# Kernel optimization log

Hardware: AMD Instinct MI355X
Metric: run time of the kernel (lower is better)

Reference implementation:

```python
import jax, jax.numpy as jnp
import numpy as np

EPS = 1e-5
K = 1  # kernel_size; forced to 1 by the module's channel bookkeeping (see notes)


def conv2d(x, w, stride=1, padding=0):
    return jax.lax.conv_general_dilated(
        x, w, (stride, stride), [(padding, padding), (padding, padding)],
        dimension_numbers=('NCHW', 'OIHW', 'NCHW'))


def bn_eval(x, g, b):
    # eval-mode BatchNorm2d with running_mean=0, running_var=1
    scale = g * np.float32(1.0 / np.sqrt(1.0 + EPS))
    return x * scale.reshape(1, -1, 1, 1) + b.reshape(1, -1, 1, 1)


def spdconv(x, w, g, b):
    # SPDConv: 2x2 space-to-depth -> conv (bias=False) -> BN -> SiLU
    s2d = jnp.concatenate([x[..., ::2, ::2], x[..., 1::2, ::2],
                           x[..., ::2, 1::2], x[..., 1::2, 1::2]], axis=1)
    return jax.nn.silu(bn_eval(conv2d(s2d, w), g, b))


def fourier_split(x):
    # Fourierforward(J=1): zero-pad to next pow2, rfft2, split low/high bands
    h, w = x.shape[-2], x.shape[-1]
    ph = 1 << int(np.ceil(np.log2(h)))
    pw = 1 << int(np.ceil(np.log2(w)))
    xp = jnp.pad(x, ((0, 0), (0, 0), (0, ph - h), (0, pw - w)))
    f = jnp.fft.rfft2(xp)
    low = f[:, :, :h // 2 + 1, :w // 2 + 1]
    high = f[:, :, h // 2 + 1:h + 1, :w // 2 + 1]
    return low.real, low.imag, high.real, high.imag


def sdi(x, w, b):
    # SDI1: per-sample (unbatched) 3x3 conv, then cumulative product over the batch dim
    y = conv2d(x, w, padding=1) + b.reshape(1, -1, 1, 1)
    return jnp.cumprod(y, axis=0)


def fourier_sdi(x, sdi_w, sdi_b, fuse_w, fuse_g, fuse_b):
    yl, y1, y2, y3 = fourier_split(x)
    parts = [sdi(t, sdi_w, sdi_b) for t in (yl, y1, y2, y3)]
    cat = jnp.concatenate(parts, axis=1)  # (b, 4, h', w')
    return jax.nn.silu(bn_eval(conv2d(cat, fuse_w), fuse_g, fuse_b))


def _forward(x, w_spd_gw, bn_g_gw, bn_b_gw, sdi_w_gw, sdi_b_gw, fuse_w_gw, fuse_g_gw, fuse_b_gw,
             w_spd_gf, bn_g_gf, bn_b_gf, sdi_w_gf, sdi_b_gf, fuse_w_gf, fuse_g_gf, fuse_b_gf,
             gen_g, gen_b, w_final):
    b, c = x.shape[0], x.shape[1]
    # get_weight branch: SPDConv(1x1) -> Fourier_SDIModel
    weight = fourier_sdi(spdconv(x, w_spd_gw, bn_g_gw, bn_b_gw),
                         sdi_w_gw, sdi_b_gw, fuse_w_gw, fuse_g_gw, fuse_b_gw)
    h, w = weight.shape[2], weight.shape[3]
    weighted = jax.nn.softmax(weight.reshape(b, c * c, K * K, h, w), axis=2)
    # generate_feature branch: SPDConv(k) -> Fourier_SDIModel -> BN -> ReLU
    feat = fourier_sdi(spdconv(x, w_spd_gf, bn_g_gf, bn_b_gf),
                       sdi_w_gf, sdi_b_gf, fuse_w_gf, fuse_g_gf, fuse_b_gf)
    feat = jax.nn.relu(bn_eval(feat, gen_g, gen_b)).reshape(b, c * c, K * K, h, w)
    wd = feat * weighted
    # rearrange 'b c (n1 n2) h w -> b c (h n1) (w n2)'
    conv_data = wd.reshape(b, c * c, K, K, h, w).transpose(0, 1, 4, 2, 5, 3)
    conv_data = conv_data.reshape(b, c * c, h * K, w * K)
    # final conv: kernel K, stride autopad(K, p=K)=K (passed as stride arg), no bias
    return conv2d(conv_data, w_final, stride=K)


def setup_inputs() -> dict:
    key = jax.random.key(0)
    ks = jax.random.split(key, 24)
    n = lambda i, shape, s=1.0: jax.random.normal(ks[i], shape, dtype=jnp.float32) * s
    # sdi 3x3 weights scaled ~1/(fft_magnitude*taps) so the cumulative product over
    # the batch dim stays in fp32 range.
    return {
        'x': n(0, (16, 1, 1022, 1022)),
        'w_spd_gw': n(1, (1, 4, 1, 1), 0.5),
        'bn_g_gw': 1.0 + n(2, (1,), 0.1),
        'bn_b_gw': n(3, (1,), 0.1),
        'sdi_w_gw': n(4, (1, 1, 3, 3), 5e-4),
        'sdi_b_gw': n(5, (1,), 0.01),
        'fuse_w_gw': n(6, (1, 4, 1, 1), 0.3),
        'fuse_g_gw': 1.0 + n(7, (1,), 0.1),
        'fuse_b_gw': n(8, (1,), 0.1),
        'w_spd_gf': n(9, (1, 4, 1, 1), 0.5),
        'bn_g_gf': 1.0 + n(10, (1,), 0.1),
        'bn_b_gf': n(11, (1,), 0.1),
        'sdi_w_gf': n(12, (1, 1, 3, 3), 5e-4),
        'sdi_b_gf': n(13, (1,), 0.01),
        'fuse_w_gf': n(14, (1, 4, 1, 1), 0.3),
        'fuse_g_gf': 1.0 + n(15, (1,), 0.1),
        'fuse_b_gf': n(16, (1,), 0.1),
        'gen_g': 1.0 + n(17, (1,), 0.1),
        'gen_b': n(18, (1,), 0.1),
        'w_final': n(19, (64, 1, 1, 1), 0.1),
    }


def reference(x, w_spd_gw, bn_g_gw, bn_b_gw, sdi_w_gw, sdi_b_gw, fuse_w_gw, fuse_g_gw, fuse_b_gw,
              w_spd_gf, bn_g_gf, bn_b_gf, sdi_w_gf, sdi_b_gf, fuse_w_gf, fuse_g_gf, fuse_b_gf,
              gen_g, gen_b, w_final):
    return _forward(x, w_spd_gw, bn_g_gw, bn_b_gw, sdi_w_gw, sdi_b_gw, fuse_w_gw, fuse_g_gw, fuse_b_gw,
                    w_spd_gf, bn_g_gf, bn_b_gf, sdi_w_gf, sdi_b_gf, fuse_w_gf, fuse_g_gf, fuse_b_gf,
                    gen_g, gen_b, w_final)
```

## Files before the change

kernel.cpp:

```cpp
#include <hip/hip_runtime.h>
#include <math.h>


#define PI_F 3.14159265358979323846f

__device__ __forceinline__ int brev9(int x) { return (int)(__brev((unsigned)x) >> 23); }

__device__ __forceinline__ void fft512_lds(float2* row, const float* twc,
                                           const float* tws, int l) {
    for (int s = 1; s <= 9; s++) {
        int half = 1 << (s - 1);
        int m = half << 1;
#pragma unroll
        for (int n = 0; n < 4; n++) {
            int bt  = n * 64 + l;
            int grp = bt >> (s - 1);
            int pos = bt & (half - 1);
            int i0  = grp * m + pos;
            int i1  = i0 + half;
            int ti  = pos << (9 - s);
            float cs = twc[ti], sn = tws[ti];
            float2 u = row[i0], v = row[i1];
            float tr  = v.x * cs - v.y * sn;
            float tim = v.x * sn + v.y * cs;
            row[i0] = make_float2(u.x + tr,  u.y + tim);
            row[i1] = make_float2(u.x - tr,  u.y - tim);
        }
        __syncthreads();
    }
}

__global__ __launch_bounds__(512) void fft_rows_spd(
        const float* __restrict__ x, const float* __restrict__ w4,
        const float* __restrict__ g1, const float* __restrict__ b1,
        float2* __restrict__ RT) {
    __shared__ float2 s[8][513];
    __shared__ float twc[256];
    __shared__ float tws[256];
    int t = threadIdx.x;
    if (t < 256) {
        float ang = -2.0f * PI_F * (float)t / 512.0f;
        float sn, cs; sincosf(ang, &sn, &cs);
        twc[t] = cs; tws[t] = sn;
    }
    int w = t >> 6, l = t & 63;
    int row = blockIdx.x * 8 + w;
    int b = row >> 9, yy = row & 511;
    float w0 = w4[0], w1 = w4[1], w2 = w4[2], w3 = w4[3];
    float scale = g1[0] * rsqrtf(1.0f + 1e-5f);
    float bias  = b1[0];
#pragma unroll
    for (int n = 0; n < 8; n++) {
        int p = n * 64 + l;
        float v = 0.f;
        if (yy < 511 && p < 511) {
            const float* r0 = x + ((size_t)b * 1022 + 2 * yy) * 1022 + 2 * p;
            float2 e = *(const float2*)r0;
            float2 o = *(const float2*)(r0 + 1022);
            v = w0 * e.x + w1 * o.x + w2 * e.y + w3 * o.y;
            v = v * scale + bias;
            v = v / (1.0f + expf(-v));
        }
        s[w][brev9(p)] = make_float2(v, 0.f);
    }
    __syncthreads();
    fft512_lds(s[w], twc, tws, l);
    int k = t >> 1, sub = t & 1;
    int y0 = (blockIdx.x & 63) * 8;
    float2* dst = RT + ((size_t)(b * 256 + k)) * 512 + y0 + sub * 4;
#pragma unroll
    for (int r = 0; r < 4; r++) dst[r] = s[sub * 4 + r][k];
}

__global__ __launch_bounds__(512) void fft_cols_k(
        const float2* __restrict__ RT, float* __restrict__ tpl) {
    __shared__ float2 s[8][513];
    __shared__ float twc[256];
    __shared__ float tws[256];
    int t = threadIdx.x;
    if (t < 256) {
        float ang = -2.0f * PI_F * (float)t / 512.0f;
        float sn, cs; sincosf(ang, &sn, &cs);
        twc[t] = cs; tws[t] = sn;
    }
    int w = t >> 6, l = t & 63;
    int b = blockIdx.x >> 5;
    int kx0 = (blockIdx.x & 31) * 8;
    const float2* src = RT + ((size_t)(b * 256 + kx0 + w)) * 512;
#pragma unroll
    for (int n = 0; n < 8; n++) {
        int yv = n * 64 + l;
        s[w][brev9(yv)] = src[yv];
    }
    __syncthreads();
    fft512_lds(s[w], twc, tws, l);
    const size_t plane = (size_t)16 * 256 * 256;
    int kx_off = t & 7;
    int kyg = t >> 3;
#pragma unroll
    for (int p = 0; p < 4; p++) {
        int ky = p * 64 + kyg;
        float2 lo = s[kx_off][ky];
        float2 hi = s[kx_off][ky + 256];
        size_t off = ((size_t)(b * 256 + ky)) * 256 + kx0 + kx_off;
        tpl[off]             = lo.x;
        tpl[plane + off]     = lo.y;
        tpl[2 * plane + off] = hi.x;
        tpl[3 * plane + off] = hi.y;
    }
}

__global__ void conv_y_k(const float* __restrict__ tpl,
                         const float* __restrict__ sdiw,
                         const float* __restrict__ sdib,
                         float* __restrict__ y) {
    int idx = blockIdx.x * 256 + threadIdx.x;
    int j = idx & 255, i = (idx >> 8) & 255;
    const float* base = tpl + ((size_t)(idx >> 16)) * 65536;
    float acc = sdib[0];
    float w9[9];
#pragma unroll
    for (int k = 0; k < 9; k++) w9[k] = sdiw[k];
#pragma unroll
    for (int di = 0; di < 3; di++) {
        int ii = i + di - 1;
        if (ii < 0 || ii > 255) continue;
        const float* rowp = base + (size_t)ii * 256;
#pragma unroll
        for (int dj = 0; dj < 3; dj++) {
            int jj = j + dj - 1;
            if (jj < 0 || jj > 255) continue;
            acc += w9[di * 3 + dj] * rowp[jj];
        }
    }
    y[idx] = acc;
}

__global__ void cum_fuse_k(const float* __restrict__ y,
                           const float* __restrict__ fw,
                           const float* __restrict__ fg,
                           const float* __restrict__ fb,
                           const float* __restrict__ gg,
                           const float* __restrict__ gb,
                           float* __restrict__ feat2) {
    int pix = blockIdx.x * 256 + threadIdx.x;
    float v[16][4];
#pragma unroll
    for (int b = 0; b < 16; b++)
#pragma unroll
        for (int c = 0; c < 4; c++)
            v[b][c] = y[((size_t)(c * 16 + b)) * 65536 + pix];
    float inv = rsqrtf(1.0f + 1e-5f);
    float fscale = fg[0] * inv, fbias = fb[0];
    float gscale = gg[0] * inv, gbias = gb[0];
    float fw0 = fw[0], fw1 = fw[1], fw2 = fw[2], fw3 = fw[3];
    float p0 = 1.f, p1 = 1.f, p2 = 1.f, p3 = 1.f;
#pragma unroll
    for (int b = 0; b < 16; b++) {
        p0 *= v[b][0]; p1 *= v[b][1]; p2 *= v[b][2]; p3 *= v[b][3];
        float f = fw0 * p0 + fw1 * p1 + fw2 * p2 + fw3 * p3;
        float bnv = f * fscale + fbias;
        float feat = bnv / (1.0f + expf(-bnv));
        float f2 = feat * gscale + gbias;
        f2 = fmaxf(f2, 0.f);
        feat2[(size_t)b * 65536 + pix] = f2;
    }
}

__global__ void expand_out(const float* __restrict__ feat2,
                           const float* __restrict__ wf,
                           float* __restrict__ out) {
    int tid = blockIdx.x * 256 + threadIdx.x;
    int j4 = tid & 63;
    int i  = (tid >> 6) & 255;
    int b  = tid >> 14;
    const float4 v = *(const float4*)(feat2 + (((size_t)b * 256 + i) * 256 + j4 * 4));
    float* obase = out + (size_t)b * 64 * 65536 + (size_t)i * 256 + j4 * 4;
#pragma unroll
    for (int o = 0; o < 64; o++) {
        float sC = wf[o];
        float4 r = make_float4(v.x * sC, v.y * sC, v.z * sC, v.w * sC);
        *(float4*)(obase + (size_t)o * 65536) = r;
    }
}

extern "C" void kernel_launch(void* const* d_in, const int* in_sizes, int n_in,
                              void* d_out, int out_size, void* d_ws, size_t ws_size,
                              hipStream_t stream) {
    const float* x    = (const float*)d_in[0];
    const float* wspd = (const float*)d_in[9];
    const float* bng  = (const float*)d_in[10];
    const float* bnb  = (const float*)d_in[11];
    const float* sdiw = (const float*)d_in[12];
    const float* sdib = (const float*)d_in[13];
    const float* fw   = (const float*)d_in[14];
    const float* fg   = (const float*)d_in[15];
    const float* fb   = (const float*)d_in[16];
    const float* gg   = (const float*)d_in[17];
    const float* gb   = (const float*)d_in[18];
    const float* wf   = (const float*)d_in[19];
    float* out = (float*)d_out;

    float2* RT    = (float2*)d_ws;
    float*  tpl   = (float*)d_ws + (size_t)4 * 1024 * 1024;
    float*  y     = (float*)d_ws;
    float*  feat2 = tpl;

    fft_rows_spd<<<dim3(1024),  dim3(512), 0, stream>>>(x, wspd, bng, bnb, RT);
    fft_cols_k  <<<dim3(512),   dim3(512), 0, stream>>>(RT, tpl);
    conv_y_k    <<<dim3(16384), dim3(256), 0, stream>>>(tpl, sdiw, sdib, y);
    cum_fuse_k  <<<dim3(256),   dim3(256), 0, stream>>>(y, fw, fg, fb, gg, gb, feat2);
    expand_out  <<<dim3(1024),  dim3(256), 0, stream>>>(feat2, wf, out);
}
```

Baseline: 414.2 us.

## Use register radix-8 FFT and fuse cumulative product with output expansion

Replaces the LDS-based radix-2 512-point FFT (nine barrier-separated stages, with twiddle tables) with a three-pass radix-8 decomposition. Butterflies run in registers, twiddles come from sincosf, and only two LDS transposes are needed. The FFT outputs are staged through a padded shared tile so global stores are more contiguous. The cumulative-product/fuse kernel is merged with the 64-channel output expansion, which removes the intermediate feat2 buffer and one launch. The catch is that the fused kernel writes with only one float per thread per row, at 256-pixel granularity across 512 blocks, which may reduce store efficiency and parallelism for the dominant 268MB output write.

```diff
diff --git a/kernel.cpp b/kernel.cpp
--- a/kernel.cpp
+++ b/kernel.cpp
@@ -4,109 +4,168 @@
 
 #define PI_F 3.14159265358979323846f
 
-__device__ __forceinline__ int brev9(int x) { return (int)(__brev((unsigned)x) >> 23); }
-
-__device__ __forceinline__ void fft512_lds(float2* row, const float* twc,
-                                           const float* tws, int l) {
-    for (int s = 1; s <= 9; s++) {
-        int half = 1 << (s - 1);
-        int m = half << 1;
-#pragma unroll
-        for (int n = 0; n < 4; n++) {
-            int bt  = n * 64 + l;
-            int grp = bt >> (s - 1);
-            int pos = bt & (half - 1);
-            int i0  = grp * m + pos;
-            int i1  = i0 + half;
-            int ti  = pos << (9 - s);
-            float cs = twc[ti], sn = tws[ti];
-            float2 u = row[i0], v = row[i1];
-            float tr  = v.x * cs - v.y * sn;
-            float tim = v.x * sn + v.y * cs;
-            row[i0] = make_float2(u.x + tr,  u.y + tim);
-            row[i1] = make_float2(u.x - tr,  u.y - tim);
-        }
-        __syncthreads();
-    }
-}
-
-__global__ __launch_bounds__(512) void fft_rows_spd(
+struct cpx { float re, im; };
+__device__ __forceinline__ cpx cadd(cpx a, cpx b){ return {a.re+b.re, a.im+b.im}; }
+__device__ __forceinline__ cpx csub(cpx a, cpx b){ return {a.re-b.re, a.im-b.im}; }
+__device__ __forceinline__ cpx cmul(cpx a, cpx b){ return {a.re*b.re - a.im*b.im, a.re*b.im + a.im*b.re}; }
+__device__ __forceinline__ cpx cnegi(cpx a){ return {a.im, -a.re}; }
+
+__device__ __forceinline__ void dft8_dif(cpx* a) {
+    const float C = 0.70710678118654752440f;
+    cpx t0=cadd(a[0],a[4]), t1=cadd(a[1],a[5]), t2=cadd(a[2],a[6]), t3=cadd(a[3],a[7]);
+    cpx s0=csub(a[0],a[4]), s1=csub(a[1],a[5]), s2=csub(a[2],a[6]), s3=csub(a[3],a[7]);
+    s1 = (cpx){ C*(s1.re + s1.im), C*(s1.im - s1.re) };
+    s2 = cnegi(s2);
+    s3 = (cpx){ C*(s3.im - s3.re), -C*(s3.re + s3.im) };
+    cpx u0=cadd(t0,t2), u1=cadd(t1,t3), u2=csub(t0,t2), u3=cnegi(csub(t1,t3));
+    cpx v0=cadd(s0,s2), v1=cadd(s1,s3), v2=csub(s0,s2), v3=cnegi(csub(s1,s3));
+    a[0]=cadd(u0,u1); a[1]=csub(u0,u1); a[2]=cadd(u2,u3); a[3]=csub(u2,u3);
+    a[4]=cadd(v0,v1); a[5]=csub(v0,v1); a[6]=cadd(v2,v3); a[7]=csub(v2,v3);
+}
+
+__device__ __forceinline__ void twiddle_brev(cpx* a, cpx p) {
+    cpx w = p;
+    a[4] = cmul(a[4], w); w = cmul(w, p);
+    a[2] = cmul(a[2], w); w = cmul(w, p);
+    a[6] = cmul(a[6], w); w = cmul(w, p);
+    a[1] = cmul(a[1], w); w = cmul(w, p);
+    a[5] = cmul(a[5], w); w = cmul(w, p);
+    a[3] = cmul(a[3], w); w = cmul(w, p);
+    a[7] = cmul(a[7], w);
+}
+
+__device__ __forceinline__ void fft512_r8(cpx* a, float* bR, float* bI, int t) {
+    float sn, cs;
+    dft8_dif(a);
+    sincosf(-2.0f * PI_F * (float)t / 512.0f, &sn, &cs);
+    twiddle_brev(a, (cpx){cs, sn});
+    bR[0*69 + t] = a[0].re; bI[0*69 + t] = a[0].im;
+    bR[4*69 + t] = a[1].re; bI[4*69 + t] = a[1].im;
+    bR[2*69 + t] = a[2].re; bI[2*69 + t] = a[2].im;
+    bR[6*69 + t] = a[3].re; bI[6*69 + t] = a[3].im;
+    bR[1*69 + t] = a[4].re; bI[1*69 + t] = a[4].im;
+    bR[5*69 + t] = a[5].re; bI[5*69 + t] = a[5].im;
+    bR[3*69 + t] = a[6].re; bI[3*69 + t] = a[6].im;
+    bR[7*69 + t] = a[7].re; bI[7*69 + t] = a[7].im;
+    __syncthreads();
+    int k0 = t & 7, t0 = t >> 3;
+    cpx b[8];
+#pragma unroll
+    for (int i = 0; i < 8; i++) {
+        b[i].re = bR[k0*69 + t0 + 8*i];
+        b[i].im = bI[k0*69 + t0 + 8*i];
+    }
+    __syncthreads();
+    dft8_dif(b);
+    sincosf(-2.0f * PI_F * (float)t0 / 64.0f, &sn, &cs);
+    twiddle_brev(b, (cpx){cs, sn});
+    bR[(0*8 + k0)*9 + t0] = b[0].re; bI[(0*8 + k0)*9 + t0] = b[0].im;
+    bR[(4*8 + k0)*9 + t0] = b[1].re; bI[(4*8 + k0)*9 + t0] = b[1].im;
+    bR[(2*8 + k0)*9 + t0] = b[2].re; bI[(2*8 + k0)*9 + t0] = b[2].im;
+    bR[(6*8 + k0)*9 + t0] = b[3].re; bI[(6*8 + k0)*9 + t0] = b[3].im;
+    bR[(1*8 + k0)*9 + t0] = b[4].re; bI[(1*8 + k0)*9 + t0] = b[4].im;
+    bR[(5*8 + k0)*9 + t0] = b[5].re; bI[(5*8 + k0)*9 + t0] = b[5].im;
+    bR[(3*8 + k0)*9 + t0] = b[6].re; bI[(3*8 + k0)*9 + t0] = b[6].im;
+    bR[(7*8 + k0)*9 + t0] = b[7].re; bI[(7*8 + k0)*9 + t0] = b[7].im;
+    __syncthreads();
+    int rowb = ((t >> 3) * 8 + (t & 7)) * 9;
+#pragma unroll
+    for (int i = 0; i < 8; i++) {
+        a[i].re = bR[rowb + i];
+        a[i].im = bI[rowb + i];
+    }
+    __syncthreads();
+    dft8_dif(a);
+}
+
+__global__ __launch_bounds__(512) void fft_rows_spd8(
         const float* __restrict__ x, const float* __restrict__ w4,
         const float* __restrict__ g1, const float* __restrict__ b1,
         float2* __restrict__ RT) {
-    __shared__ float2 s[8][513];
-    __shared__ float twc[256];
-    __shared__ float tws[256];
-    int t = threadIdx.x;
-    if (t < 256) {
-        float ang = -2.0f * PI_F * (float)t / 512.0f;
-        float sn, cs; sincosf(ang, &sn, &cs);
-        twc[t] = cs; tws[t] = sn;
-    }
-    int w = t >> 6, l = t & 63;
+    __shared__ __align__(16) float pool[9216];
+    int tid = threadIdx.x;
+    int w = tid >> 6, t = tid & 63;
+    float* bR = pool + w * 1152;
+    float* bI = bR + 576;
     int row = blockIdx.x * 8 + w;
     int b = row >> 9, yy = row & 511;
-    float w0 = w4[0], w1 = w4[1], w2 = w4[2], w3 = w4[3];
-    float scale = g1[0] * rsqrtf(1.0f + 1e-5f);
+    float w0 = w4[0], w1 = w4[1], w2c = w4[2], w3 = w4[3];
+    float scale = g1[0] * rsqrtf(1.f + 1e-5f);
     float bias  = b1[0];
-#pragma unroll
-    for (int n = 0; n < 8; n++) {
-        int p = n * 64 + l;
+    cpx a[8];
+#pragma unroll
+    for (int m = 0; m < 8; m++) {
+        int p = t + 64 * m;
         float v = 0.f;
         if (yy < 511 && p < 511) {
             const float* r0 = x + ((size_t)b * 1022 + 2 * yy) * 1022 + 2 * p;
             float2 e = *(const float2*)r0;
             float2 o = *(const float2*)(r0 + 1022);
-            v = w0 * e.x + w1 * o.x + w2 * e.y + w3 * o.y;
+            v = w0 * e.x + w1 * o.x + w2c * e.y + w3 * o.y;
             v = v * scale + bias;
-            v = v / (1.0f + expf(-v));
+            v = v / (1.f + expf(-v));
         }
-        s[w][brev9(p)] = make_float2(v, 0.f);
-    }
-    __syncthreads();
-    fft512_lds(s[w], twc, tws, l);
-    int k = t >> 1, sub = t & 1;
+        a[m] = (cpx){v, 0.f};
+    }
+    fft512_r8(a, bR, bI, t);
+    float2* tile = (float2*)pool;
+    tile[(t +   0) * 9 + w] = make_float2(a[0].re, a[0].im);
+    tile[(t +  64) * 9 + w] = make_float2(a[4].re, a[4].im);
+    tile[(t + 128) * 9 + w] = make_float2(a[2].re, a[2].im);
+    tile[(t + 192) * 9 + w] = make_float2(a[6].re, a[6].im);
+    __syncthreads();
     int y0 = (blockIdx.x & 63) * 8;
-    float2* dst = RT + ((size_t)(b * 256 + k)) * 512 + y0 + sub * 4;
-#pragma unroll
-    for (int r = 0; r < 4; r++) dst[r] = s[sub * 4 + r][k];
-}
-
-__global__ __launch_bounds__(512) void fft_cols_k(
+    float2* dst = RT + (size_t)(b * 256) * 512 + y0;
+#pragma unroll
+    for (int r = 0; r < 4; r++) {
+        int e = tid + 512 * r;
+        int k = e >> 3, ww = e & 7;
+        dst[(size_t)k * 512 + ww] = tile[k * 9 + ww];
+    }
+}
+
+__global__ __launch_bounds__(512) void fft_cols8(
         const float2* __restrict__ RT, float* __restrict__ tpl) {
-    __shared__ float2 s[8][513];
-    __shared__ float twc[256];
-    __shared__ float tws[256];
-    int t = threadIdx.x;
-    if (t < 256) {
-        float ang = -2.0f * PI_F * (float)t / 512.0f;
-        float sn, cs; sincosf(ang, &sn, &cs);
-        twc[t] = cs; tws[t] = sn;
-    }
-    int w = t >> 6, l = t & 63;
+    __shared__ __align__(16) float pool[9216];
+    int tid = threadIdx.x;
+    int w = tid >> 6, t = tid & 63;
+    float* bR = pool + w * 1152;
+    float* bI = bR + 576;
     int b = blockIdx.x >> 5;
     int kx0 = (blockIdx.x & 31) * 8;
-    const float2* src = RT + ((size_t)(b * 256 + kx0 + w)) * 512;
-#pragma unroll
-    for (int n = 0; n < 8; n++) {
-        int yv = n * 64 + l;
-        s[w][brev9(yv)] = src[yv];
-    }
-    __syncthreads();
-    fft512_lds(s[w], twc, tws, l);
-    const size_t plane = (size_t)16 * 256 * 256;
-    int kx_off = t & 7;
-    int kyg = t >> 3;
-#pragma unroll
-    for (int p = 0; p < 4; p++) {
-        int ky = p * 64 + kyg;
-        float2 lo = s[kx_off][ky];
-        float2 hi = s[kx_off][ky + 256];
-        size_t off = ((size_t)(b * 256 + ky)) * 256 + kx0 + kx_off;
-        tpl[off]             = lo.x;
-        tpl[plane + off]     = lo.y;
-        tpl[2 * plane + off] = hi.x;
-        tpl[3 * plane + off] = hi.y;
+    const float2* src = RT + (size_t)(b * 256 + kx0 + w) * 512;
+    cpx a[8];
+#pragma unroll
+    for (int m = 0; m < 8; m++) {
+        float2 v = src[t + 64 * m];
+        a[m] = (cpx){v.x, v.y};
+    }
+    fft512_r8(a, bR, bI, t);
+    float2* tile = (float2*)pool;
+    tile[(t +   0) * 9 + w] = make_float2(a[0].re, a[0].im);
+    tile[(t +  64) * 9 + w] = make_float2(a[4].re, a[4].im);
+    tile[(t + 128) * 9 + w] = make_float2(a[2].re, a[2].im);
+    tile[(t + 192) * 9 + w] = make_float2(a[6].re, a[6].im);
+    tile[(t + 256) * 9 + w] = make_float2(a[1].re, a[1].im);
+    tile[(t + 320) * 9 + w] = make_float2(a[5].re, a[5].im);
+    tile[(t + 384) * 9 + w] = make_float2(a[3].re, a[3].im);
+    tile[(t + 448) * 9 + w] = make_float2(a[7].re, a[7].im);
+    __syncthreads();
+    const size_t P = (size_t)16 * 256 * 256;
+#pragma unroll
+    for (int r = 0; r < 8; r++) {
+        int e = tid + 512 * r;
+        int ky = e >> 3, ww = e & 7;
+        float2 v = tile[ky * 9 + ww];
+        if (ky < 256) {
+            size_t idx = (size_t)(b * 256 + ky) * 256 + kx0 + ww;
+            tpl[idx]     = v.x;
+            tpl[P + idx] = v.y;
+        } else {
+            size_t idx = (size_t)(b * 256 + (ky - 256)) * 256 + kx0 + ww;
+            tpl[2*P + idx] = v.x;
+            tpl[3*P + idx] = v.y;
+        }
     }
 }
 
@@ -136,51 +195,41 @@
     y[idx] = acc;
 }
 
-__global__ void cum_fuse_k(const float* __restrict__ y,
-                           const float* __restrict__ fw,
-                           const float* __restrict__ fg,
-                           const float* __restrict__ fb,
-                           const float* __restrict__ gg,
-                           const float* __restrict__ gb,
-                           float* __restrict__ feat2) {
-    int pix = blockIdx.x * 256 + threadIdx.x;
+__global__ __launch_bounds__(256) void cum_expand(
+        const float* __restrict__ y,
+        const float* __restrict__ fw, const float* __restrict__ fg,
+        const float* __restrict__ fb, const float* __restrict__ gg,
+        const float* __restrict__ gb, const float* __restrict__ wf,
+        float* __restrict__ out) {
+    int og = blockIdx.x & 1;
+    int pix = (blockIdx.x >> 1) * 256 + threadIdx.x;
     float v[16][4];
 #pragma unroll
     for (int b = 0; b < 16; b++)
 #pragma unroll
         for (int c = 0; c < 4; c++)
             v[b][c] = y[((size_t)(c * 16 + b)) * 65536 + pix];
-    float inv = rsqrtf(1.0f + 1e-5f);
+    float inv = rsqrtf(1.f + 1e-5f);
     float fscale = fg[0] * inv, fbias = fb[0];
     float gscale = gg[0] * inv, gbias = gb[0];
     float fw0 = fw[0], fw1 = fw[1], fw2 = fw[2], fw3 = fw[3];
+    float f2[16];
     float p0 = 1.f, p1 = 1.f, p2 = 1.f, p3 = 1.f;
 #pragma unroll
     for (int b = 0; b < 16; b++) {
         p0 *= v[b][0]; p1 *= v[b][1]; p2 *= v[b][2]; p3 *= v[b][3];
         float f = fw0 * p0 + fw1 * p1 + fw2 * p2 + fw3 * p3;
-        float bnv = f * fscale + fbias;
-        float feat = bnv / (1.0f + expf(-bnv));
-        float f2 = feat * gscale + gbias;
-        f2 = fmaxf(f2, 0.f);
-        feat2[(size_t)b * 65536 + pix] = f2;
-    }
-}
-
-__global__ void expand_out(const float* __restrict__ feat2,
-                           const float* __restrict__ wf,
-                           float* __restrict__ out) {
-    int tid = blockIdx.x * 256 + threadIdx.x;
-    int j4 = tid & 63;
-    int i  = (tid >> 6) & 255;
-    int b  = tid >> 14;
-    const float4 v = *(const float4*)(feat2 + (((size_t)b * 256 + i) * 256 + j4 * 4));
-    float* obase = out + (size_t)b * 64 * 65536 + (size_t)i * 256 + j4 * 4;
-#pragma unroll
-    for (int o = 0; o < 64; o++) {
-        float sC = wf[o];
-        float4 r = make_float4(v.x * sC, v.y * sC, v.z * sC, v.w * sC);
-        *(float4*)(obase + (size_t)o * 65536) = r;
+        float bn = f * fscale + fbias;
+        float ft = bn / (1.f + expf(-bn));
+        float g = ft * gscale + gbias;
+        f2[b] = fmaxf(g, 0.f);
+    }
+    for (int oo = 0; oo < 32; oo++) {
+        int o = og * 32 + oo;
+        float s = wf[o];
+#pragma unroll
+        for (int b = 0; b < 16; b++)
+            out[((size_t)(b * 64 + o)) * 65536 + pix] = f2[b] * s;
     }
 }
 
@@ -201,14 +250,12 @@
     const float* wf   = (const float*)d_in[19];
     float* out = (float*)d_out;
 
-    float2* RT    = (float2*)d_ws;
-    float*  tpl   = (float*)d_ws + (size_t)4 * 1024 * 1024;
-    float*  y     = (float*)d_ws;
-    float*  feat2 = tpl;
-
-    fft_rows_spd<<<dim3(1024),  dim3(512), 0, stream>>>(x, wspd, bng, bnb, RT);
-    fft_cols_k  <<<dim3(512),   dim3(512), 0, stream>>>(RT, tpl);
-    conv_y_k    <<<dim3(16384), dim3(256), 0, stream>>>(tpl, sdiw, sdib, y);
-    cum_fuse_k  <<<dim3(256),   dim3(256), 0, stream>>>(y, fw, fg, fb, gg, gb, feat2);
-    expand_out  <<<dim3(1024),  dim3(256), 0, stream>>>(feat2, wf, out);
-}
+    float2* RT  = (float2*)d_ws;
+    float*  tpl = (float*)d_ws + (size_t)4 * 1024 * 1024;
+    float*  y   = (float*)d_ws;
+
+    fft_rows_spd8<<<dim3(1024),  dim3(512), 0, stream>>>(x, wspd, bng, bnb, RT);
+    fft_cols8    <<<dim3(512),   dim3(512), 0, stream>>>(RT, tpl);
+    conv_y_k     <<<dim3(16384), dim3(256), 0, stream>>>(tpl, sdiw, sdib, y);
+    cum_expand   <<<dim3(512),   dim3(256), 0, stream>>>(y, fw, fg, fb, gg, gb, wf, out);
+}
```

Measured after the change: 400.0 us. 3.4% less time.
